# Kernel optimization log

Hardware: AMD Instinct MI355X
Metric: run time of the kernel (lower is better)

The kernel has to match this reference:

```python
import jax, jax.numpy as jnp
import numpy as np

B, L, V, E, H, T = 32, 512, 100000, 300, 256, 4  # H = hidden_dim//2 per direction


def setup_inputs() -> dict:
    key = jax.random.key(0)
    ks = jax.random.split(key, 16)
    word_ids = jax.random.randint(ks[0], (B, L), 0, V, dtype=jnp.int32)
    mask = jnp.ones((B, L), dtype=jnp.int32)
    label_ids = jax.random.randint(ks[1], (B, L), 0, T, dtype=jnp.int32)
    emb = jax.random.uniform(ks[2], (V, E), minval=-0.25, maxval=0.25, dtype=jnp.float32)
    emb = emb.at[0].set(0.0)  # padding_idx=0
    w = lambda k, s: jax.random.normal(k, s, dtype=jnp.float32) * 0.05
    return {
        "word_ids": word_ids, "mask": mask, "label_ids": label_ids,
        "emb": emb,
        "Wih_f": w(ks[3], (4 * H, E)), "Whh_f": w(ks[4], (4 * H, H)), "b_f": jnp.zeros((4 * H,), jnp.float32),
        "Wih_b": w(ks[5], (4 * H, E)), "Whh_b": w(ks[6], (4 * H, H)), "b_b": jnp.zeros((4 * H,), jnp.float32),
        "W_out": w(ks[7], (T, 2 * H)), "b_out": jnp.zeros((T,), jnp.float32),
        "transitions": w(ks[8], (T, T)), "start_trans": w(ks[9], (T,)), "end_trans": w(ks[10], (T,)),
    }


def _lstm_dir(x, Wih, Whh, b):
    # x: [B, L, E] -> hs: [B, L, H]; PyTorch gate order i, f, g, o
    xg = jnp.einsum('ble,ge->blg', x, Wih) + b  # [B, L, 4H]
    h0 = jnp.zeros((x.shape[0], Whh.shape[1]), x.dtype)

    def step(carry, g):
        h, c = carry
        gates = g + h @ Whh.T
        i, f, gg, o = jnp.split(gates, 4, axis=-1)
        c = jax.nn.sigmoid(f) * c + jax.nn.sigmoid(i) * jnp.tanh(gg)
        h = jax.nn.sigmoid(o) * jnp.tanh(c)
        return (h, c), h

    _, hs = jax.lax.scan(step, (h0, h0), jnp.swapaxes(xg, 0, 1))
    return jnp.swapaxes(hs, 0, 1)


def _emissions(word_ids, emb, Wih_f, Whh_f, b_f, Wih_b, Whh_b, b_b, W_out, b_out):
    x = emb[word_ids]                                   # [B, L, E]
    h_fwd = _lstm_dir(x, Wih_f, Whh_f, b_f)
    h_bwd = _lstm_dir(x[:, ::-1], Wih_b, Whh_b, b_b)[:, ::-1]
    h = jnp.concatenate([h_fwd, h_bwd], axis=-1)        # [B, L, 2H]
    return h @ W_out.T + b_out                          # [B, L, T]


def _viterbi_decode(emissions, mask, transitions, start_trans, end_trans):
    m = mask.astype(bool)
    score0 = start_trans + emissions[:, 0]              # [B, T]

    def step(score, inp):
        emit_t, mask_t = inp                            # [B,T], [B]
        cand = score[:, :, None] + transitions[None] + emit_t[:, None, :]  # [B, T_from, T_to]
        idx = jnp.argmax(cand, axis=1).astype(jnp.int32)
        new = jnp.max(cand, axis=1)
        return jnp.where(mask_t[:, None], new, score), idx

    score, history = jax.lax.scan(
        step, score0,
        (jnp.swapaxes(emissions[:, 1:], 0, 1), jnp.swapaxes(m[:, 1:], 0, 1)))
    score = score + end_trans
    last_tag = jnp.argmax(score, axis=-1).astype(jnp.int32)  # [B]

    def back(tag, inp):
        idx_t, mask_t = inp
        prev = jnp.take_along_axis(idx_t, tag[:, None], axis=1)[:, 0]
        tag = jnp.where(mask_t, prev, tag)
        return tag, tag

    _, tags_rev = jax.lax.scan(back, last_tag,
                               (history, jnp.swapaxes(m[:, 1:], 0, 1)), reverse=True)
    tags = jnp.concatenate([jnp.swapaxes(tags_rev, 0, 1), last_tag[:, None]], axis=1)  # [B, L]
    return tags * mask.astype(jnp.int32)  # zero out padding like torch y_pred init


def reference(word_ids, mask, label_ids, emb, Wih_f, Whh_f, b_f, Wih_b, Whh_b, b_b,
              W_out, b_out, transitions, start_trans, end_trans):
    emissions = _emissions(word_ids, emb, Wih_f, Whh_f, b_f, Wih_b, Whh_b, b_b, W_out, b_out)
    return _viterbi_decode(emissions, mask, transitions, start_trans, end_trans)
```

## Files before the change

kernel.cpp:

```cpp
#include <hip/hip_runtime.h>
#include <math.h>

#define B_   32
#define L_   512
#define E_   300
#define H_   256
#define T_   4
#define NTOK 16384
#define XGLD 2048
#define SENT 2.0f

typedef float f32x4 __attribute__((ext_vector_type(4)));
typedef float f32x2 __attribute__((ext_vector_type(2)));

__device__ __forceinline__ float fsigmoid_(float x) { return 1.0f / (1.0f + __expf(-x)); }
__device__ __forceinline__ float ftanh_(float x) {
  return 1.0f - 2.0f / (__expf(2.0f * x) + 1.0f);
}

__device__ __forceinline__ void llc_store_f32(float* p, float v) {
  asm volatile("global_store_dword %0, %1, off sc0 sc1" :: "v"(p), "v"(v) : "memory");
}
__device__ __forceinline__ void llc_store_f32x4(float* p, f32x4 v) {
  asm volatile("global_store_dwordx4 %0, %1, off sc0 sc1" :: "v"(p), "v"(v) : "memory");
}
__device__ __forceinline__ f32x4 llc_load_f32x4(const float* p) {
  f32x4 r;
  asm volatile("global_load_dwordx4 %0, %1, off sc0 sc1" : "=&v"(r) : "v"(p) : "memory");
  return r;
}

#define XBM 128
#define XBN 128
#define XBK 20
__global__ __launch_bounds__(256) void xproj_kernel(
    const int*   __restrict__ wid,
    const float* __restrict__ emb,
    const float* __restrict__ wih_f,
    const float* __restrict__ wih_b,
    const float* __restrict__ b_f,
    const float* __restrict__ b_b,
    float* __restrict__ xg,
    float*       h_all,
    int          n4)
{
  __shared__ float Ast[XBK][XBM];
  __shared__ float Bst[XBK][XBN];
  __shared__ int   wid_s[XBM];

  const int tid = threadIdx.x;
  const int m0 = blockIdx.y * XBM;
  const int n0 = blockIdx.x * XBN;
  const int d  = n0 >> 10;
  const float* wih  = d ? wih_b : wih_f;
  const float* bias = d ? b_b  : b_f;
  const int g0 = n0 & 1023;

  if (tid < XBM) wid_s[tid] = wid[m0 + tid];
  __syncthreads();

  const int srow = tid & 127;
  const int half = tid >> 7;
  const float* sbase = half ? (wih + (size_t)(g0 + srow) * E_)
                            : (emb + (size_t)wid_s[srow] * E_);
  float* sdst = half ? &Bst[0][0] : &Ast[0][0];

  f32x4 pre[5];
#pragma unroll
  for (int qd = 0; qd < 5; ++qd) pre[qd] = *(const f32x4*)(sbase + qd * 4);

  const int tx = tid & 15, ty = tid >> 4;
  float acc[8][8] = {};

  for (int k0 = 0; k0 < 300; k0 += XBK) {
#pragma unroll
    for (int qd = 0; qd < 5; ++qd)
#pragma unroll
      for (int e = 0; e < 4; ++e)
        sdst[(qd * 4 + e) * XBM + srow] = pre[qd][e];
    if (k0 + XBK < 300) {
      const float* p = sbase + k0 + XBK;
#pragma unroll
      for (int qd = 0; qd < 5; ++qd) pre[qd] = *(const f32x4*)(p + qd * 4);
    }
    __syncthreads();

#pragma unroll
    for (int k = 0; k < XBK; ++k) {
      float av[8], bv[8];
      *(f32x4*)&av[0] = *(const f32x4*)&Ast[k][ty * 8];
      *(f32x4*)&av[4] = *(const f32x4*)&Ast[k][ty * 8 + 4];
      *(f32x4*)&bv[0] = *(const f32x4*)&Bst[k][tx * 8];
      *(f32x4*)&bv[4] = *(const f32x4*)&Bst[k][tx * 8 + 4];
#pragma unroll
      for (int i = 0; i < 8; ++i)
#pragma unroll
        for (int j = 0; j < 8; ++j)
          acc[i][j] += av[i] * bv[j];
    }
    __syncthreads();
  }

#pragma unroll
  for (int i = 0; i < 8; ++i) {
    const int r = m0 + ty * 8 + i;
    float* op = xg + (size_t)r * XGLD + n0 + tx * 8;
#pragma unroll
    for (int j = 0; j < 8; ++j)
      op[j] = acc[i][j] + bias[g0 + tx * 8 + j];
  }

  {
    const int blin = blockIdx.y * 16 + blockIdx.x;
    f32x4 sv = {SENT, SENT, SENT, SENT};
    for (int i = blin * 256 + tid; i < n4; i += 2048 * 256)
      llc_store_f32x4(h_all + (size_t)i * 4, sv);
  }
}

__global__ __launch_bounds__(512, 2) void lstm_kernel(
    const float* __restrict__ xg,
    const float* __restrict__ whh_f,
    const float* __restrict__ whh_b,
    float*       h_all)
{
  const int bid = blockIdx.x;
  const int d   = bid >> 7;
  const int q   = (bid >> 4) & 7;
  const int sl  = bid & 15;
  const int tid = threadIdx.x;
  const int kp  = tid >> 6;
  const int lane = tid & 63;
  const int bl_loc = lane >> 5;
  const int rg  = lane & 31;
  const float* __restrict__ whh = d ? whh_b : whh_f;

  __shared__ float h_lds[4 * 260];
  __shared__ float part_lds[2 * 8 * 2 * 72];

  f32x4 wreg[2][8];
#pragma unroll
  for (int r = 0; r < 2; ++r) {
    const int row_l = rg * 2 + r;
    const int u  = row_l >> 2;
    const int gt = row_l & 3;
    const int grow = gt * 256 + sl * 16 + u;
    const float* rp = whh + (size_t)grow * H_ + kp * 32;
#pragma unroll
    for (int qq = 0; qq < 8; ++qq) wreg[r][qq] = *(const f32x4*)(rp + qq * 4);
  }

  for (int idx = tid; idx < 4 * 260; idx += 512) h_lds[idx] = 0.f;
  __syncthreads();

  float* hgrp = h_all + (size_t)(d * 8 + q) * (L_ * 1024);

  const int r_u  = (tid & 31) >> 1;
  const int r_bl = (tid < 32) ? (tid & 1) : (2 + (tid & 1));
  float c = 0.f;
  const float* xbase = xg + ((size_t)(q * 4 + r_bl) * L_) * XGLD + d * 1024 + sl * 16 + r_u;
  float x0 = 0.f, x1 = 0.f, x2 = 0.f, x3 = 0.f;
  if (tid < 64) {
    const int t0 = d ? (L_ - 1) : 0;
    const float* xp = xbase + (size_t)t0 * XGLD;
    x0 = xp[0]; x1 = xp[256]; x2 = xp[512]; x3 = xp[768];
  }

#define GEMM_PHASE(PH, BLBASE)                                                \
  do {                                                                        \
    const int blg = (BLBASE) + bl_loc;                                        \
    const float* hb = &h_lds[blg * 260 + kp * 32];                            \
    float a0 = 0.f, a1 = 0.f;                                                 \
    _Pragma("unroll")                                                         \
    for (int i = 0; i < 8; ++i) {                                             \
      f32x4 hv = *(const f32x4*)(hb + i * 4);                                 \
      a0 += wreg[0][i].x * hv.x + wreg[0][i].y * hv.y                         \
          + wreg[0][i].z * hv.z + wreg[0][i].w * hv.w;                        \
      a1 += wreg[1][i].x * hv.x + wreg[1][i].y * hv.y                         \
          + wreg[1][i].z * hv.z + wreg[1][i].w * hv.w;                        \
    }                                                                         \
    f32x2 pv = {a0, a1};                                                      \
    *(f32x2*)&part_lds[(PH) * 1152 + kp * 144 + bl_loc * 72 + rg * 2] = pv;   \
  } while (0)

#define REDUCE_PUBLISH(PH, TT, TN)                                            \
  do {                                                                        \
    f32x4 g = {x0, x1, x2, x3};                                               \
    _Pragma("unroll")                                                         \
    for (int k2 = 0; k2 < 8; ++k2)                                            \
      g += *(const f32x4*)&part_lds[(PH) * 1152 + k2 * 144                    \
                                    + (tid & 1) * 72 + r_u * 4];              \
    float gi = fsigmoid_(g.x);                                                \
    float gf = fsigmoid_(g.y);                                                \
    float gg = ftanh_(g.z);                                                   \
    float go = fsigmoid_(g.w);                                                \
    c = gf * c + gi * gg;                                                     \
    float h = go * ftanh_(c);                                                 \
    llc_store_f32(&hgrp[(size_t)(TT) * 1024 + r_bl * 256 + sl * 16 + r_u], h);\
    if ((TN) >= 0) {                                                          \
      const float* xp = xbase + (size_t)(TN) * XGLD;                          \
      x0 = xp[0]; x1 = xp[256]; x2 = xp[512]; x3 = xp[768];                   \
    }                                                                         \
  } while (0)

#define SPIN_LOAD(BLBASE, TT)                                                 \
  do {                                                                        \
    const int i = tid - 64;                                                   \
    const int blg = (BLBASE) + (i >> 6);                                      \
    const int j4 = (i & 63) * 4;                                              \
    const float* p0 = hgrp + (size_t)(TT) * 1024 + blg * 256 + j4;            \
    f32x4 v0;                                                                 \
    bool bad;                                                                 \
    do {                                                                      \
      v0 = llc_load_f32x4(p0);                                                \
      asm volatile("s_waitcnt vmcnt(0)" ::: "memory");                        \
      __builtin_amdgcn_sched_barrier(0);                                      \
      bad = (v0.x == SENT) | (v0.y == SENT) | (v0.z == SENT) | (v0.w == SENT);\
    } while (bad);                                                            \
    *(f32x4*)&h_lds[blg * 260 + j4] = v0;                                     \
  } while (0)

  for (int s = 0; s < L_; ++s) {
    const int t  = d ? (L_ - 1 - s) : s;
    const int tp = d ? (t + 1) : (t - 1);
    const int tn = (s < L_ - 1) ? (d ? (t - 1) : (t + 1)) : -1;

    GEMM_PHASE(0, 0);
    __syncthreads();

    if (tid < 32) {
      REDUCE_PUBLISH(0, t, tn);
    } else if (s > 0 && tid >= 64 && tid < 192) {
      SPIN_LOAD(2, tp);
    }
    __syncthreads();

    GEMM_PHASE(1, 2);
    __syncthreads();

    if (tid >= 32 && tid < 64) {
      REDUCE_PUBLISH(1, t, tn);
    } else if (s < L_ - 1 && tid >= 64 && tid < 192) {
      SPIN_LOAD(0, t);
    }
    __syncthreads();
  }

#undef GEMM_PHASE
#undef REDUCE_PUBLISH
#undef SPIN_LOAD
}

__global__ __launch_bounds__(512) void emvit_kernel(
    const float* __restrict__ h_all,
    const float* __restrict__ wout,
    const float* __restrict__ bout,
    const float* __restrict__ trans,
    const float* __restrict__ strans,
    const float* __restrict__ etrans,
    const int*   __restrict__ mask,
    int* __restrict__ out)
{
  __shared__ float em_l[512 * 4];
  __shared__ float wsl[2048];
  __shared__ int   msk_l[512];
  __shared__ int   hist_l[512 * 4];
  __shared__ int   tags_l[512];

  const int b = blockIdx.x;
  const int q = b >> 2, blq = b & 3;
  const int tid = threadIdx.x;
  const float* hfp = h_all + (size_t)(0 + q) * (L_ * 1024) + blq * 256;
  const float* hbp = h_all + (size_t)(8 + q) * (L_ * 1024) + blq * 256;

  for (int i = tid; i < 2048; i += 512) wsl[i] = wout[i];
  if (tid < 512) msk_l[tid] = mask[b * L_ + tid];
  __syncthreads();

  const int tw = tid >> 6, lane = tid & 63;
  const float bo0 = bout[0], bo1 = bout[1], bo2 = bout[2], bo3 = bout[3];
  for (int tt = tw; tt < L_; tt += 8) {
    const float* hf = hfp + (size_t)tt * 1024;
    const float* hb = hbp + (size_t)tt * 1024;
    float s0 = 0.f, s1 = 0.f, s2 = 0.f, s3 = 0.f;
#pragma unroll
    for (int i = 0; i < 4; ++i) {
      const int j = i * 64 + lane;
      const float hfv = hf[j], hbv = hb[j];
      s0 += hfv * wsl[j]        + hbv * wsl[256 + j];
      s1 += hfv * wsl[512 + j]  + hbv * wsl[768 + j];
      s2 += hfv * wsl[1024 + j] + hbv * wsl[1280 + j];
      s3 += hfv * wsl[1536 + j] + hbv * wsl[1792 + j];
    }
#pragma unroll
    for (int m = 1; m < 64; m <<= 1) {
      s0 += __shfl_xor(s0, m, 64);
      s1 += __shfl_xor(s1, m, 64);
      s2 += __shfl_xor(s2, m, 64);
      s3 += __shfl_xor(s3, m, 64);
    }
    if (lane == 0) {
      em_l[tt * 4 + 0] = s0 + bo0;
      em_l[tt * 4 + 1] = s1 + bo1;
      em_l[tt * 4 + 2] = s2 + bo2;
      em_l[tt * 4 + 3] = s3 + bo3;
    }
  }
  __syncthreads();

  if (tid == 0) {
    float tr[4][4];
#pragma unroll
    for (int i = 0; i < 4; ++i)
#pragma unroll
      for (int jj = 0; jj < 4; ++jj) tr[i][jj] = trans[i * 4 + jj];

    float sc[4];
#pragma unroll
    for (int tag = 0; tag < 4; ++tag) sc[tag] = strans[tag] + em_l[tag];

    for (int t = 1; t < L_; ++t) {
      float ns[4];
#pragma unroll
      for (int to = 0; to < 4; ++to) {
        float best = sc[0] + tr[0][to];
        int bf = 0;
#pragma unroll
        for (int fr = 1; fr < 4; ++fr) {
          float v = sc[fr] + tr[fr][to];
          if (v > best) { best = v; bf = fr; }
        }
        ns[to] = best + em_l[t * 4 + to];
        hist_l[t * 4 + to] = bf;
      }
      const int mt = msk_l[t];
#pragma unroll
      for (int to = 0; to < 4; ++to) sc[to] = mt ? ns[to] : sc[to];
    }

#pragma unroll
    for (int tag = 0; tag < 4; ++tag) sc[tag] += etrans[tag];
    int cur = 0;
    float best = sc[0];
#pragma unroll
    for (int i = 1; i < 4; ++i)
      if (sc[i] > best) { best = sc[i]; cur = i; }

    tags_l[L_ - 1] = msk_l[L_ - 1] ? cur : 0;
    for (int t = L_ - 1; t >= 1; --t) {
      if (msk_l[t]) cur = hist_l[t * 4 + cur];
      tags_l[t - 1] = msk_l[t - 1] ? cur : 0;
    }
  }
  __syncthreads();
  if (tid < 512) out[b * L_ + tid] = tags_l[tid];
}

extern "C" void kernel_launch(void* const* d_in, const int* in_sizes, int n_in,
                              void* d_out, int out_size, void* d_ws, size_t ws_size,
                              hipStream_t stream) {
  const int*   word_ids = (const int*)d_in[0];
  const int*   mask     = (const int*)d_in[1];
  const float* emb   = (const float*)d_in[3];
  const float* Wih_f = (const float*)d_in[4];
  const float* Whh_f = (const float*)d_in[5];
  const float* b_f   = (const float*)d_in[6];
  const float* Wih_b = (const float*)d_in[7];
  const float* Whh_b = (const float*)d_in[8];
  const float* b_b   = (const float*)d_in[9];
  const float* W_out = (const float*)d_in[10];
  const float* b_out = (const float*)d_in[11];
  const float* trans = (const float*)d_in[12];
  const float* strans = (const float*)d_in[13];
  const float* etrans = (const float*)d_in[14];
  int* out = (int*)d_out;

  float* xg    = (float*)d_ws;
  float* h_all = xg + (size_t)NTOK * XGLD;

  const int n4 = 16 * L_ * 1024 / 4;
  xproj_kernel<<<dim3(16, 128), 256, 0, stream>>>(word_ids, emb, Wih_f, Wih_b,
                                                  b_f, b_b, xg, h_all, n4);
  lstm_kernel<<<256, 512, 0, stream>>>(xg, Whh_f, Whh_b, h_all);
  emvit_kernel<<<32, 512, 0, stream>>>(h_all, W_out, b_out, trans, strans,
                                       etrans, mask, out);
}
```

Before: 1.099 ms.

## Fuse emission projection into LSTM recurrence using idle threads of slice-0 blocks

Blocks with sl==0 use their otherwise idle threads (tid>=256) to compute per-direction partial emission dot products from the h vectors already staged in LDS each step, writing them to a small em_part buffer. The separate emission kernel, which reread all of h_all from memory, is replaced by a small 64-thread Viterbi kernel that only sums the forward and backward partials plus bias. The final timestep needs an extra spin-load and emit pass after the loop. This adds work inside the latency-critical recurrence loop of some blocks and may lengthen their per-step critical path.

```diff
diff --git a/kernel.cpp b/kernel.cpp
--- a/kernel.cpp
+++ b/kernel.cpp
@@ -122,7 +122,9 @@
     const float* __restrict__ xg,
     const float* __restrict__ whh_f,
     const float* __restrict__ whh_b,
-    float*       h_all)
+    const float* __restrict__ wout,
+    float*       h_all,
+    float*       em_part)
 {
   const int bid = blockIdx.x;
   const int d   = bid >> 7;
@@ -137,6 +139,7 @@
 
   __shared__ float h_lds[4 * 260];
   __shared__ float part_lds[2 * 8 * 2 * 72];
+  __shared__ float wsl_l[1024];
 
   f32x4 wreg[2][8];
 #pragma unroll
@@ -151,6 +154,8 @@
   }
 
   for (int idx = tid; idx < 4 * 260; idx += 512) h_lds[idx] = 0.f;
+  for (int idx = tid; idx < 1024; idx += 512)
+    wsl_l[idx] = wout[(idx >> 8) * 512 + d * 256 + (idx & 255)];
   __syncthreads();
 
   float* hgrp = h_all + (size_t)(d * 8 + q) * (L_ * 1024);
@@ -203,9 +208,9 @@
     }                                                                         \
   } while (0)
 
-#define SPIN_LOAD(BLBASE, TT)                                                 \
+#define SPIN_LOAD(BASETID, BLBASE, TT)                                        \
   do {                                                                        \
-    const int i = tid - 64;                                                   \
+    const int i = tid - (BASETID);                                            \
     const int blg = (BLBASE) + (i >> 6);                                      \
     const int j4 = (i & 63) * 4;                                              \
     const float* p0 = hgrp + (size_t)(TT) * 1024 + blg * 256 + j4;            \
@@ -220,6 +225,26 @@
     *(f32x4*)&h_lds[blg * 260 + j4] = v0;                                     \
   } while (0)
 
+#define EMIT(BLBASE, TT)                                                      \
+  do {                                                                        \
+    const int e   = tid - 256;                                                \
+    const int tag = e >> 6;                                                   \
+    const int l   = e & 63;                                                   \
+    const int blp = l >> 5;                                                   \
+    const int li  = l & 31;                                                   \
+    const int blg = (BLBASE) + blp;                                           \
+    float sacc = 0.f;                                                         \
+    _Pragma("unroll")                                                         \
+    for (int i8 = 0; i8 < 8; ++i8) {                                          \
+      const int j = li + 32 * i8;                                             \
+      sacc += h_lds[blg * 260 + j] * wsl_l[tag * 256 + j];                    \
+    }                                                                         \
+    _Pragma("unroll")                                                         \
+    for (int m = 1; m < 32; m <<= 1) sacc += __shfl_xor(sacc, m, 64);         \
+    if (li == 0)                                                              \
+      em_part[(((size_t)d * 32 + q * 4 + blg) * L_ + (TT)) * 4 + tag] = sacc; \
+  } while (0)
+
   for (int s = 0; s < L_; ++s) {
     const int t  = d ? (L_ - 1 - s) : s;
     const int tp = d ? (t + 1) : (t - 1);
@@ -231,7 +256,9 @@
     if (tid < 32) {
       REDUCE_PUBLISH(0, t, tn);
     } else if (s > 0 && tid >= 64 && tid < 192) {
-      SPIN_LOAD(2, tp);
+      SPIN_LOAD(64, 2, tp);
+    } else if (sl == 0 && s > 0 && tid >= 256) {
+      EMIT(0, tp);
     }
     __syncthreads();
 
@@ -241,19 +268,32 @@
     if (tid >= 32 && tid < 64) {
       REDUCE_PUBLISH(1, t, tn);
     } else if (s < L_ - 1 && tid >= 64 && tid < 192) {
-      SPIN_LOAD(0, t);
-    }
-    __syncthreads();
+      SPIN_LOAD(64, 0, t);
+    } else if (sl == 0 && s > 0 && tid >= 256) {
+      EMIT(2, tp);
+    }
+    __syncthreads();
+  }
+
+  if (sl == 0) {
+    const int tl = d ? 0 : (L_ - 1);
+    if (tid >= 64 && tid < 192) SPIN_LOAD(64, 0, tl);
+    else if (tid >= 192 && tid < 320) SPIN_LOAD(192, 2, tl);
+    __syncthreads();
+    if (tid >= 256) {
+      EMIT(0, tl);
+      EMIT(2, tl);
+    }
   }
 
 #undef GEMM_PHASE
 #undef REDUCE_PUBLISH
 #undef SPIN_LOAD
-}
-
-__global__ __launch_bounds__(512) void emvit_kernel(
-    const float* __restrict__ h_all,
-    const float* __restrict__ wout,
+#undef EMIT
+}
+
+__global__ __launch_bounds__(64) void viterbi_kernel(
+    const float* __restrict__ em_part,
     const float* __restrict__ bout,
     const float* __restrict__ trans,
     const float* __restrict__ strans,
@@ -262,49 +302,21 @@
     int* __restrict__ out)
 {
   __shared__ float em_l[512 * 4];
-  __shared__ float wsl[2048];
   __shared__ int   msk_l[512];
   __shared__ int   hist_l[512 * 4];
   __shared__ int   tags_l[512];
 
   const int b = blockIdx.x;
-  const int q = b >> 2, blq = b & 3;
   const int tid = threadIdx.x;
-  const float* hfp = h_all + (size_t)(0 + q) * (L_ * 1024) + blq * 256;
-  const float* hbp = h_all + (size_t)(8 + q) * (L_ * 1024) + blq * 256;
-
-  for (int i = tid; i < 2048; i += 512) wsl[i] = wout[i];
-  if (tid < 512) msk_l[tid] = mask[b * L_ + tid];
-  __syncthreads();
-
-  const int tw = tid >> 6, lane = tid & 63;
-  const float bo0 = bout[0], bo1 = bout[1], bo2 = bout[2], bo3 = bout[3];
-  for (int tt = tw; tt < L_; tt += 8) {
-    const float* hf = hfp + (size_t)tt * 1024;
-    const float* hb = hbp + (size_t)tt * 1024;
-    float s0 = 0.f, s1 = 0.f, s2 = 0.f, s3 = 0.f;
-#pragma unroll
-    for (int i = 0; i < 4; ++i) {
-      const int j = i * 64 + lane;
-      const float hfv = hf[j], hbv = hb[j];
-      s0 += hfv * wsl[j]        + hbv * wsl[256 + j];
-      s1 += hfv * wsl[512 + j]  + hbv * wsl[768 + j];
-      s2 += hfv * wsl[1024 + j] + hbv * wsl[1280 + j];
-      s3 += hfv * wsl[1536 + j] + hbv * wsl[1792 + j];
-    }
-#pragma unroll
-    for (int m = 1; m < 64; m <<= 1) {
-      s0 += __shfl_xor(s0, m, 64);
-      s1 += __shfl_xor(s1, m, 64);
-      s2 += __shfl_xor(s2, m, 64);
-      s3 += __shfl_xor(s3, m, 64);
-    }
-    if (lane == 0) {
-      em_l[tt * 4 + 0] = s0 + bo0;
-      em_l[tt * 4 + 1] = s1 + bo1;
-      em_l[tt * 4 + 2] = s2 + bo2;
-      em_l[tt * 4 + 3] = s3 + bo3;
-    }
+  const float* epf = em_part + ((size_t)(0 + b) * L_) * 4;
+  const float* epb = em_part + ((size_t)(32 + b) * L_) * 4;
+  const f32x4 bo4 = {bout[0], bout[1], bout[2], bout[3]};
+
+  for (int i = tid; i < 512; i += 64) {
+    f32x4 e0 = *(const f32x4*)&epf[i * 4];
+    f32x4 e1 = *(const f32x4*)&epb[i * 4];
+    *(f32x4*)&em_l[i * 4] = e0 + e1 + bo4;
+    msk_l[i] = mask[b * L_ + i];
   }
   __syncthreads();
 
@@ -353,7 +365,7 @@
     }
   }
   __syncthreads();
-  if (tid < 512) out[b * L_ + tid] = tags_l[tid];
+  for (int i = tid; i < 512; i += 64) out[b * L_ + i] = tags_l[i];
 }
 
 extern "C" void kernel_launch(void* const* d_in, const int* in_sizes, int n_in,
@@ -375,13 +387,14 @@
   const float* etrans = (const float*)d_in[14];
   int* out = (int*)d_out;
 
-  float* xg    = (float*)d_ws;
-  float* h_all = xg + (size_t)NTOK * XGLD;
+  float* xg      = (float*)d_ws;
+  float* h_all   = xg + (size_t)NTOK * XGLD;
+  float* em_part = h_all + (size_t)16 * L_ * 1024;
 
   const int n4 = 16 * L_ * 1024 / 4;
   xproj_kernel<<<dim3(16, 128), 256, 0, stream>>>(word_ids, emb, Wih_f, Wih_b,
                                                   b_f, b_b, xg, h_all, n4);
-  lstm_kernel<<<256, 512, 0, stream>>>(xg, Whh_f, Whh_b, h_all);
-  emvit_kernel<<<32, 512, 0, stream>>>(h_all, W_out, b_out, trans, strans,
-                                       etrans, mask, out);
-}
+  lstm_kernel<<<256, 512, 0, stream>>>(xg, Whh_f, Whh_b, W_out, h_all, em_part);
+  viterbi_kernel<<<32, 64, 0, stream>>>(em_part, b_out, trans, strans, etrans,
+                                        mask, out);
+}
```

New measurement: 1.046 ms. 4.8% less time.
